# Kernel tuning notes

Hardware: AMD Instinct MI355X
Metric: run time of the kernel (lower is better)

Reference implementation:

```python
import jax, jax.numpy as jnp
import numpy as np

NUM_TAGS = 128
VOCAB = 50257
SEQ_LEN = 8192
START_TAG = 0   # tag2id['<s>'] in the original
END_TAG = 1     # vocab['</s>'] in the original (code quirk; treated as end-tag id)
NEG_INF = -10000.0


def setup_inputs() -> dict:
    key = jax.random.key(0)
    k1, k2, k3 = jax.random.split(key, 3)
    x = jax.random.randint(k1, (SEQ_LEN,), 0, VOCAB)
    emit_score = jax.random.normal(k2, (VOCAB, NUM_TAGS), dtype=jnp.float32)
    transitions = jax.random.normal(k3, (NUM_TAGS, NUM_TAGS), dtype=jnp.float32)
    return {"x": x, "emit_score": emit_score, "transitions": transitions}


def reference(x, emit_score, transitions):
    # CRF forward algorithm (log partition function z).
    # Original: per-timestep, per-tag python loops of log_sum_exp over
    # _score = alphas[:, None] + emit[ch_id][None, :] + transitions.
    # All num_tags updates at step t read the *old* alphas (the in-place
    # writes only touch _score's source after it was built), so this is the
    # standard vectorized recurrence: a logsumexp reduction over the prev-tag axis.
    emits = emit_score[x[1:]]  # [S-1, T] gathered emission scores
    init_alphas = jnp.full((NUM_TAGS,), NEG_INF, dtype=emit_score.dtype).at[START_TAG].set(0.0)

    def step(alphas, emit_t):
        # score[prev, cur] = alphas[prev] + emit_t[cur] + transitions[prev, cur]
        score = alphas[:, None] + emit_t[None, :] + transitions  # [T, T]
        return jax.nn.logsumexp(score, axis=0), None

    alphas, _ = jax.lax.scan(step, init_alphas, emits)
    z = jax.nn.logsumexp(alphas + transitions[:, END_TAG])  # scalar
    return z
```

## Files before the change

kernel.cpp:

```cpp
#include <hip/hip_runtime.h>

#define NTG 128
#define NSTEPS 8191
#define GCH 512
#define LCH 16
#define MATF16 (NTG*NTG)

typedef _Float16 half8v  __attribute__((ext_vector_type(8)));
typedef _Float16 half4v  __attribute__((ext_vector_type(4)));
typedef float    float4v __attribute__((ext_vector_type(4)));

__device__ __forceinline__ int su(int row, int col){
  return (row*NTG + col) ^ ((row & 15) << 3);
}

__device__ __forceinline__ float wave_max(float v){
#pragma unroll
  for (int m = 32; m >= 1; m >>= 1) v = fmaxf(v, __shfl_xor(v, m));
  return v;
}
__device__ __forceinline__ float wave_sum(float v){
#pragma unroll
  for (int m = 32; m >= 1; m >>= 1) v += __shfl_xor(v, m);
  return v;
}

__global__ __launch_bounds__(256, 2)
void k_chunks(const int* __restrict__ x, const float* __restrict__ emit,
              const float* __restrict__ T, _Float16* __restrict__ Pn,
              _Float16* __restrict__ Pt, double* __restrict__ scale)
{
  __shared__ _Float16 X[MATF16];
  __shared__ float red_g[2][4];

  const int t = threadIdx.x;
  const int lane = t & 63, wv = t >> 6;
  const int l15 = lane & 15, g4 = lane >> 4;
  const int g = blockIdx.x;
  const int s0 = g*LCH;
  const int nst = min(LCH, NSTEPS - s0);

  half8v aE[2][4];
#pragma unroll
  for (int jt=0; jt<2; ++jt){
    const int j = (wv*2+jt)*16 + l15;
#pragma unroll
    for (int ks=0; ks<4; ++ks){
      half8v a;
#pragma unroll
      for (int jj=0; jj<8; ++jj)
        a[jj] = (_Float16)__expf(T[(ks*32 + g4*8 + jj)*NTG + j]);
      aE[jt][ks] = a;
    }
  }

  double cacc;
  {
    const int tok = x[1+s0];
    const float* er = emit + (size_t)tok*NTG;
    const float2 me2 = *(const float2*)(er + lane*2);
    const float m0 = wave_max(fmaxf(me2.x, me2.y));
    const float sa = __expf(me2.x - m0) * 0.0078125f;
    const float sb = __expf(me2.y - m0) * 0.0078125f;
    const int j0 = lane*2;
    for (int it2=0; it2<32; ++it2){
      const int idx = it2*256 + t;
      const int i = idx >> 6;
      const float2 tv = *(const float2*)(T + (size_t)i*NTG + j0);
      union { unsigned int u; _Float16 h[2]; } pk;
      pk.h[0] = (_Float16)(__expf(tv.x)*sa);
      pk.h[1] = (_Float16)(__expf(tv.y)*sb);
      *(unsigned int*)&X[su(i, j0)] = pk.u;
    }
    cacc = (double)m0 + 4.852030263919617;
  }
  __syncthreads();

  float pscale = 1.0f;
  float4v accv[2][8];
  for (int s=1; s<nst; ++s){
    const int tok = x[1+s0+s];
    const float* er = emit + (size_t)tok*NTG;
    const float2 me2 = *(const float2*)(er + lane*2);
    const float m = wave_max(fmaxf(me2.x, me2.y));
    float ehp[2][4];
#pragma unroll
    for (int jt=0; jt<2; ++jt)
#pragma unroll
      for (int r=0; r<4; ++r)
        ehp[jt][r] = __expf(er[(wv*2+jt)*16 + g4*4 + r] - m) * pscale;

#pragma unroll
    for (int jt=0; jt<2; ++jt)
#pragma unroll
      for (int it=0; it<8; ++it) accv[jt][it] = (float4v){0.f,0.f,0.f,0.f};

#pragma unroll
    for (int it=0; it<8; ++it){
      const int c = it*16 + l15;
      half8v bf[4];
#pragma unroll
      for (int ks=0; ks<4; ++ks)
        bf[ks] = *(const half8v*)&X[su(c, ks*32 + g4*8)];
#pragma unroll
      for (int jt=0; jt<2; ++jt)
#pragma unroll
        for (int ks=0; ks<4; ++ks)
          accv[jt][it] = __builtin_amdgcn_mfma_f32_16x16x32_f16(aE[jt][ks], bf[ks], accv[jt][it], 0,0,0);
    }

    float gm = 0.f;
#pragma unroll
    for (int jt=0; jt<2; ++jt)
#pragma unroll
      for (int it=0; it<8; ++it)
#pragma unroll
        for (int r=0;r<4;r++){
          const float v = accv[jt][it][r]*ehp[jt][r];
          accv[jt][it][r] = v;
          gm = fmaxf(gm, v);
        }
    __syncthreads();
#pragma unroll
    for (int jt=0; jt<2; ++jt)
#pragma unroll
      for (int it=0; it<8; ++it){
        half4v h;
#pragma unroll
        for (int r=0;r<4;r++) h[r] = (_Float16)accv[jt][it][r];
        *(half4v*)&X[su(it*16 + l15, (wv*2+jt)*16 + g4*4)] = h;
      }
    gm = wave_max(gm);
    if (lane==0) red_g[s&1][wv] = gm;
    __syncthreads();
    const float gmax = fmaxf(fmaxf(red_g[s&1][0],red_g[s&1][1]),
                             fmaxf(red_g[s&1][2],red_g[s&1][3]));
    pscale = 1.0f/gmax;
    cacc += (double)m + (double)__logf(gmax);
  }

  const float inv = pscale;
  unsigned int* pn = (unsigned int*)(Pn + (size_t)g*MATF16);
  unsigned int* pt = (unsigned int*)(Pt + (size_t)g*MATF16);
  for (int it2=0; it2<32; ++it2){
    const int idx = it2*256 + t;
    const int i = idx >> 6, j0 = (t&63)*2;
    union { unsigned int u; _Float16 h[2]; } pk;
    pk.u = *(const unsigned int*)&X[su(i, j0)];
    pk.h[0] = (_Float16)((float)pk.h[0]*inv);
    pk.h[1] = (_Float16)((float)pk.h[1]*inv);
    pn[idx] = pk.u;
  }
  for (int it2=0; it2<32; ++it2){
    const int uidx = it2*256 + t;
    const int jj = uidx >> 6, ii = (t&63)*2;
    union { unsigned int u; _Float16 h[2]; } pk;
    pk.h[0] = (_Float16)((float)X[su(ii,   jj)]*inv);
    pk.h[1] = (_Float16)((float)X[su(ii+1, jj)]*inv);
    pt[uidx] = pk.u;
  }
  if (t==0) scale[g] = cacc;
}

__global__ __launch_bounds__(256, 2)
void k_comb8(const _Float16* __restrict__ Pn_in, const _Float16* __restrict__ Pt_in,
             const double* __restrict__ Sin,
             _Float16* __restrict__ Pn_out, _Float16* __restrict__ Pt_out,
             double* __restrict__ Sout)
{
  __shared__ _Float16 X[MATF16];
  __shared__ float red_g[2][4];
  const int t = threadIdx.x;
  const int lane = t & 63, wv = t >> 6;
  const int l15 = lane & 15, g4 = lane >> 4;
  const int p = blockIdx.x;

  const unsigned int* src = (const unsigned int*)(Pn_in + (size_t)p*8*MATF16);
  for (int it2=0; it2<32; ++it2){
    const int idx = it2*256 + t;
    const int i = idx >> 6, j0 = (t&63)*2;
    *(unsigned int*)&X[su(i, j0)] = src[idx];
  }
  __syncthreads();

  float pscale = 1.0f;
  double slog = 0.0;
  float4v accv[2][8];
  for (int mi=1; mi<8; ++mi){
    const _Float16* Yt = Pt_in + (size_t)(p*8+mi)*MATF16;
    half8v aB[2][4];
#pragma unroll
    for (int jt=0; jt<2; ++jt){
      const int j = (wv*2+jt)*16 + l15;
#pragma unroll
      for (int ks=0; ks<4; ++ks)
        aB[jt][ks] = *(const half8v*)(Yt + (size_t)j*NTG + ks*32 + g4*8);
    }

#pragma unroll
    for (int jt=0; jt<2; ++jt)
#pragma unroll
      for (int it=0; it<8; ++it) accv[jt][it] = (float4v){0.f,0.f,0.f,0.f};

#pragma unroll
    for (int it=0; it<8; ++it){
      const int c = it*16 + l15;
      half8v bf[4];
#pragma unroll
      for (int ks=0; ks<4; ++ks)
        bf[ks] = *(const half8v*)&X[su(c, ks*32 + g4*8)];
#pragma unroll
      for (int jt=0; jt<2; ++jt)
#pragma unroll
        for (int ks=0; ks<4; ++ks)
          accv[jt][it] = __builtin_amdgcn_mfma_f32_16x16x32_f16(aB[jt][ks], bf[ks], accv[jt][it], 0,0,0);
    }

    float gm = 0.f;
#pragma unroll
    for (int jt=0; jt<2; ++jt)
#pragma unroll
      for (int it=0; it<8; ++it)
#pragma unroll
        for (int r=0;r<4;r++){
          const float v = accv[jt][it][r]*pscale;
          accv[jt][it][r] = v;
          gm = fmaxf(gm, v);
        }
    __syncthreads();
#pragma unroll
    for (int jt=0; jt<2; ++jt)
#pragma unroll
      for (int it=0; it<8; ++it){
        half4v h;
#pragma unroll
        for (int r=0;r<4;r++) h[r] = (_Float16)accv[jt][it][r];
        *(half4v*)&X[su(it*16 + l15, (wv*2+jt)*16 + g4*4)] = h;
      }
    gm = wave_max(gm);
    if (lane==0) red_g[mi&1][wv] = gm;
    __syncthreads();
    const float gmax = fmaxf(fmaxf(red_g[mi&1][0],red_g[mi&1][1]),
                             fmaxf(red_g[mi&1][2],red_g[mi&1][3]));
    pscale = 1.0f/gmax;
    slog += (double)__logf(gmax);
  }

  const float inv = pscale;
  unsigned int* pn = (unsigned int*)(Pn_out + (size_t)p*MATF16);
  unsigned int* pt = (unsigned int*)(Pt_out + (size_t)p*MATF16);
  for (int it2=0; it2<32; ++it2){
    const int idx = it2*256 + t;
    const int i = idx >> 6, j0 = (t&63)*2;
    union { unsigned int u; _Float16 h[2]; } pk;
    pk.u = *(const unsigned int*)&X[su(i, j0)];
    pk.h[0] = (_Float16)((float)pk.h[0]*inv);
    pk.h[1] = (_Float16)((float)pk.h[1]*inv);
    pn[idx] = pk.u;
  }
  for (int it2=0; it2<32; ++it2){
    const int uidx = it2*256 + t;
    const int jj = uidx >> 6, ii = (t&63)*2;
    union { unsigned int u; _Float16 h[2]; } pk;
    pk.h[0] = (_Float16)((float)X[su(ii,   jj)]*inv);
    pk.h[1] = (_Float16)((float)X[su(ii+1, jj)]*inv);
    pt[uidx] = pk.u;
  }
  if (t==0){
    double ssum = slog;
#pragma unroll
    for (int q=0;q<8;q++) ssum += Sin[p*8+q];
    Sout[p] = ssum;
  }
}

__global__ void k_final(const _Float16* __restrict__ PtC, const double* __restrict__ scC,
                        const float* __restrict__ T, float* __restrict__ out)
{
  __shared__ float u[2][NTG];
  __shared__ float red[4], red2[4];
  const int t = threadIdx.x;
  const int lane = t & 63, wv = t >> 6;

  double acc = 0.0;
#pragma unroll
  for (int q=0;q<8;q++) acc += scC[q];

  if (t < NTG) u[0][t] = (t==0) ? 1.f : 0.f;
  __syncthreads();

  int cur = 0;
  const int r = t >> 1, off = (t&1)*64;
  for (int k=0;k<8;k++){
    const _Float16* Y = PtC + (size_t)k*MATF16 + (size_t)r*NTG + off;
    float dot = 0.f;
#pragma unroll
    for (int q=0;q<8;q++){
      const half8v h = *(const half8v*)(Y + q*8);
#pragma unroll
      for (int e=0;e<8;e++) dot += (float)h[e]*u[cur][off + q*8 + e];
    }
    dot += __shfl_xor(dot, 1);
    if ((t&1)==0) u[cur^1][r] = dot;
    __syncthreads();
    cur ^= 1;
  }

  const float val = (t < NTG) ? (__logf(u[cur][t]) + T[t*NTG + 1]) : -3.0e38f;
  float mx = wave_max(val);
  if (lane==0) red[wv] = mx;
  __syncthreads();
  mx = fmaxf(fmaxf(red[0],red[1]), fmaxf(red[2],red[3]));
  const float e = (t < NTG) ? __expf(val - mx) : 0.f;
  const float s = wave_sum(e);
  if (lane==0) red2[wv] = s;
  __syncthreads();
  if (t==0){
    const double z = (double)mx + log((double)(red2[0]+red2[1]+red2[2]+red2[3])) + acc;
    out[0] = (float)z;
  }
}

extern "C" void kernel_launch(void* const* d_in, const int* in_sizes, int n_in,
                              void* d_out, int out_size, void* d_ws, size_t ws_size,
                              hipStream_t stream)
{
  const int*   x    = (const int*)d_in[0];
  const float* emit = (const float*)d_in[1];
  const float* T    = (const float*)d_in[2];
  float* out = (float*)d_out;

  _Float16* PnA = (_Float16*)d_ws;
  _Float16* PtA = PnA + (size_t)512*MATF16;
  _Float16* PnB = PtA + (size_t)512*MATF16;
  _Float16* PtB = PnB + (size_t)64*MATF16;
  _Float16* PnC = PtB + (size_t)64*MATF16;
  _Float16* PtC = PnC + (size_t)8*MATF16;
  double* scA = (double*)(PtC + (size_t)8*MATF16);
  double* scB = scA + 512;
  double* scC = scB + 64;

  k_chunks<<<GCH, 256, 0, stream>>>(x, emit, T, PnA, PtA, scA);
  k_comb8<<<64, 256, 0, stream>>>(PnA, PtA, scA, PnB, PtB, scB);
  k_comb8<<< 8, 256, 0, stream>>>(PnB, PtB, scB, PnC, PtC, scC);
  k_final<<<1, 256, 0, stream>>>(PtC, scC, T, out);
}
```

Measured before the change: 181.3 us.

## Precompute exp(T) once, widen blocks to 512 threads, drop redundant Pn stores

Adds a prep kernel that computes exp(transitions) once in fp16, in both normal and transposed layouts, so chunk blocks load these instead of recomputing exps. Chunk and combine kernels move to 512 threads (8 waves, one 16-column tile each), which halves per-wave MFMA work and accumulator registers. The emission scale is folded into the A operand (fp16 multiply) rather than applied to accumulators. The Pn output is removed; combine kernels rebuild their initial state from the transposed Pt via a transposed LDS write. Risks include extra fp16 rounding from pre-scaling A, an added kernel launch, and bank conflicts on the transposed LDS stores.

```diff
diff --git a/kernel.cpp b/kernel.cpp
--- a/kernel.cpp
+++ b/kernel.cpp
@@ -25,13 +25,22 @@
   return v;
 }
 
-__global__ __launch_bounds__(256, 2)
+__global__ void k_prep(const float* __restrict__ T, _Float16* __restrict__ En,
+                       _Float16* __restrict__ Et){
+  const int idx = blockIdx.x*256 + threadIdx.x;
+  const int i = idx >> 7, j = idx & 127;
+  const float v = __expf(T[idx]);
+  En[idx] = (_Float16)v;
+  Et[j*NTG + i] = (_Float16)v;
+}
+
+__global__ __launch_bounds__(512, 4)
 void k_chunks(const int* __restrict__ x, const float* __restrict__ emit,
-              const float* __restrict__ T, _Float16* __restrict__ Pn,
+              const _Float16* __restrict__ Et, const _Float16* __restrict__ En,
               _Float16* __restrict__ Pt, double* __restrict__ scale)
 {
   __shared__ _Float16 X[MATF16];
-  __shared__ float red_g[2][4];
+  __shared__ float red_g[2][8];
 
   const int t = threadIdx.x;
   const int lane = t & 63, wv = t >> 6;
@@ -39,61 +48,50 @@
   const int g = blockIdx.x;
   const int s0 = g*LCH;
   const int nst = min(LCH, NSTEPS - s0);
-
-  half8v aE[2][4];
-#pragma unroll
-  for (int jt=0; jt<2; ++jt){
-    const int j = (wv*2+jt)*16 + l15;
-#pragma unroll
-    for (int ks=0; ks<4; ++ks){
-      half8v a;
-#pragma unroll
-      for (int jj=0; jj<8; ++jj)
-        a[jj] = (_Float16)__expf(T[(ks*32 + g4*8 + jj)*NTG + j]);
-      aE[jt][ks] = a;
-    }
-  }
+  const int jA = wv*16 + l15;
+
+  half8v aE[4];
+#pragma unroll
+  for (int ks=0; ks<4; ++ks)
+    aE[ks] = *(const half8v*)(Et + jA*NTG + ks*32 + g4*8);
 
   double cacc;
   {
     const int tok = x[1+s0];
     const float* er = emit + (size_t)tok*NTG;
-    const float2 me2 = *(const float2*)(er + lane*2);
+    const float2 me2 = *(const float2*)(er + (t&63)*2);
     const float m0 = wave_max(fmaxf(me2.x, me2.y));
     const float sa = __expf(me2.x - m0) * 0.0078125f;
     const float sb = __expf(me2.y - m0) * 0.0078125f;
-    const int j0 = lane*2;
-    for (int it2=0; it2<32; ++it2){
-      const int idx = it2*256 + t;
-      const int i = idx >> 6;
-      const float2 tv = *(const float2*)(T + (size_t)i*NTG + j0);
+    const int j0 = (t&63)*2;
+    const unsigned int* ens = (const unsigned int*)En;
+#pragma unroll
+    for (int it=0; it<16; ++it){
+      const int idx = it*512 + t;
       union { unsigned int u; _Float16 h[2]; } pk;
-      pk.h[0] = (_Float16)(__expf(tv.x)*sa);
-      pk.h[1] = (_Float16)(__expf(tv.y)*sb);
-      *(unsigned int*)&X[su(i, j0)] = pk.u;
+      pk.u = ens[idx];
+      pk.h[0] = (_Float16)((float)pk.h[0]*sa);
+      pk.h[1] = (_Float16)((float)pk.h[1]*sb);
+      *(unsigned int*)&X[su(idx>>6, j0)] = pk.u;
     }
     cacc = (double)m0 + 4.852030263919617;
   }
   __syncthreads();
 
   float pscale = 1.0f;
-  float4v accv[2][8];
+  float4v accv[8];
   for (int s=1; s<nst; ++s){
     const int tok = x[1+s0+s];
     const float* er = emit + (size_t)tok*NTG;
-    const float2 me2 = *(const float2*)(er + lane*2);
+    const float2 me2 = *(const float2*)(er + (t&63)*2);
     const float m = wave_max(fmaxf(me2.x, me2.y));
-    float ehp[2][4];
-#pragma unroll
-    for (int jt=0; jt<2; ++jt)
-#pragma unroll
-      for (int r=0; r<4; ++r)
-        ehp[jt][r] = __expf(er[(wv*2+jt)*16 + g4*4 + r] - m) * pscale;
-
-#pragma unroll
-    for (int jt=0; jt<2; ++jt)
-#pragma unroll
-      for (int it=0; it<8; ++it) accv[jt][it] = (float4v){0.f,0.f,0.f,0.f};
+    const _Float16 hA = (_Float16)(__expf(er[jA] - m) * pscale);
+    half8v ap[4];
+#pragma unroll
+    for (int ks=0; ks<4; ++ks) ap[ks] = aE[ks] * hA;
+
+#pragma unroll
+    for (int it=0; it<8; ++it) accv[it] = (float4v){0.f,0.f,0.f,0.f};
 
 #pragma unroll
     for (int it=0; it<8; ++it){
@@ -103,57 +101,40 @@
       for (int ks=0; ks<4; ++ks)
         bf[ks] = *(const half8v*)&X[su(c, ks*32 + g4*8)];
 #pragma unroll
-      for (int jt=0; jt<2; ++jt)
-#pragma unroll
-        for (int ks=0; ks<4; ++ks)
-          accv[jt][it] = __builtin_amdgcn_mfma_f32_16x16x32_f16(aE[jt][ks], bf[ks], accv[jt][it], 0,0,0);
+      for (int ks=0; ks<4; ++ks)
+        accv[it] = __builtin_amdgcn_mfma_f32_16x16x32_f16(ap[ks], bf[ks], accv[it], 0,0,0);
     }
 
     float gm = 0.f;
 #pragma unroll
-    for (int jt=0; jt<2; ++jt)
-#pragma unroll
-      for (int it=0; it<8; ++it)
-#pragma unroll
-        for (int r=0;r<4;r++){
-          const float v = accv[jt][it][r]*ehp[jt][r];
-          accv[jt][it][r] = v;
-          gm = fmaxf(gm, v);
-        }
-    __syncthreads();
-#pragma unroll
-    for (int jt=0; jt<2; ++jt)
-#pragma unroll
-      for (int it=0; it<8; ++it){
-        half4v h;
-#pragma unroll
-        for (int r=0;r<4;r++) h[r] = (_Float16)accv[jt][it][r];
-        *(half4v*)&X[su(it*16 + l15, (wv*2+jt)*16 + g4*4)] = h;
-      }
+    for (int it=0; it<8; ++it)
+#pragma unroll
+      for (int r=0;r<4;r++) gm = fmaxf(gm, accv[it][r]);
+    __syncthreads();
+#pragma unroll
+    for (int it=0; it<8; ++it){
+      half4v h;
+#pragma unroll
+      for (int r=0;r<4;r++) h[r] = (_Float16)accv[it][r];
+      *(half4v*)&X[su(it*16 + l15, wv*16 + g4*4)] = h;
+    }
     gm = wave_max(gm);
     if (lane==0) red_g[s&1][wv] = gm;
     __syncthreads();
-    const float gmax = fmaxf(fmaxf(red_g[s&1][0],red_g[s&1][1]),
-                             fmaxf(red_g[s&1][2],red_g[s&1][3]));
+    float gmax = red_g[s&1][0];
+#pragma unroll
+    for (int q=1;q<8;q++) gmax = fmaxf(gmax, red_g[s&1][q]);
     pscale = 1.0f/gmax;
     cacc += (double)m + (double)__logf(gmax);
   }
 
   const float inv = pscale;
-  unsigned int* pn = (unsigned int*)(Pn + (size_t)g*MATF16);
   unsigned int* pt = (unsigned int*)(Pt + (size_t)g*MATF16);
-  for (int it2=0; it2<32; ++it2){
-    const int idx = it2*256 + t;
-    const int i = idx >> 6, j0 = (t&63)*2;
-    union { unsigned int u; _Float16 h[2]; } pk;
-    pk.u = *(const unsigned int*)&X[su(i, j0)];
-    pk.h[0] = (_Float16)((float)pk.h[0]*inv);
-    pk.h[1] = (_Float16)((float)pk.h[1]*inv);
-    pn[idx] = pk.u;
-  }
-  for (int it2=0; it2<32; ++it2){
-    const int uidx = it2*256 + t;
-    const int jj = uidx >> 6, ii = (t&63)*2;
+  const int ii = (t&63)*2;
+#pragma unroll
+  for (int it=0; it<16; ++it){
+    const int uidx = it*512 + t;
+    const int jj = uidx >> 6;
     union { unsigned int u; _Float16 h[2]; } pk;
     pk.h[0] = (_Float16)((float)X[su(ii,   jj)]*inv);
     pk.h[1] = (_Float16)((float)X[su(ii+1, jj)]*inv);
@@ -162,45 +143,45 @@
   if (t==0) scale[g] = cacc;
 }
 
-__global__ __launch_bounds__(256, 2)
-void k_comb8(const _Float16* __restrict__ Pn_in, const _Float16* __restrict__ Pt_in,
-             const double* __restrict__ Sin,
-             _Float16* __restrict__ Pn_out, _Float16* __restrict__ Pt_out,
-             double* __restrict__ Sout)
+__global__ __launch_bounds__(512, 2)
+void k_comb8(const _Float16* __restrict__ Pt_in, const double* __restrict__ Sin,
+             _Float16* __restrict__ Pt_out, double* __restrict__ Sout)
 {
   __shared__ _Float16 X[MATF16];
-  __shared__ float red_g[2][4];
+  __shared__ float red_g[2][8];
   const int t = threadIdx.x;
   const int lane = t & 63, wv = t >> 6;
   const int l15 = lane & 15, g4 = lane >> 4;
   const int p = blockIdx.x;
-
-  const unsigned int* src = (const unsigned int*)(Pn_in + (size_t)p*8*MATF16);
-  for (int it2=0; it2<32; ++it2){
-    const int idx = it2*256 + t;
-    const int i = idx >> 6, j0 = (t&63)*2;
-    *(unsigned int*)&X[su(i, j0)] = src[idx];
+  const int jA = wv*16 + l15;
+
+  {
+    const unsigned int* src = (const unsigned int*)(Pt_in + (size_t)p*8*MATF16);
+    const int i0 = (t&63)*2;
+#pragma unroll
+    for (int it=0; it<16; ++it){
+      const int pos = it*512 + t;
+      union { unsigned int u; _Float16 h[2]; } pk;
+      pk.u = src[pos];
+      const int j = pos >> 6;
+      X[su(i0,   j)] = pk.h[0];
+      X[su(i0+1, j)] = pk.h[1];
+    }
   }
   __syncthreads();
 
   float pscale = 1.0f;
   double slog = 0.0;
-  float4v accv[2][8];
+  float4v accv[8];
   for (int mi=1; mi<8; ++mi){
     const _Float16* Yt = Pt_in + (size_t)(p*8+mi)*MATF16;
-    half8v aB[2][4];
-#pragma unroll
-    for (int jt=0; jt<2; ++jt){
-      const int j = (wv*2+jt)*16 + l15;
-#pragma unroll
-      for (int ks=0; ks<4; ++ks)
-        aB[jt][ks] = *(const half8v*)(Yt + (size_t)j*NTG + ks*32 + g4*8);
-    }
-
-#pragma unroll
-    for (int jt=0; jt<2; ++jt)
-#pragma unroll
-      for (int it=0; it<8; ++it) accv[jt][it] = (float4v){0.f,0.f,0.f,0.f};
+    half8v aB[4];
+#pragma unroll
+    for (int ks=0; ks<4; ++ks)
+      aB[ks] = *(const half8v*)(Yt + jA*NTG + ks*32 + g4*8);
+
+#pragma unroll
+    for (int it=0; it<8; ++it) accv[it] = (float4v){0.f,0.f,0.f,0.f};
 
 #pragma unroll
     for (int it=0; it<8; ++it){
@@ -210,57 +191,44 @@
       for (int ks=0; ks<4; ++ks)
         bf[ks] = *(const half8v*)&X[su(c, ks*32 + g4*8)];
 #pragma unroll
-      for (int jt=0; jt<2; ++jt)
-#pragma unroll
-        for (int ks=0; ks<4; ++ks)
-          accv[jt][it] = __builtin_amdgcn_mfma_f32_16x16x32_f16(aB[jt][ks], bf[ks], accv[jt][it], 0,0,0);
+      for (int ks=0; ks<4; ++ks)
+        accv[it] = __builtin_amdgcn_mfma_f32_16x16x32_f16(aB[ks], bf[ks], accv[it], 0,0,0);
     }
 
     float gm = 0.f;
 #pragma unroll
-    for (int jt=0; jt<2; ++jt)
-#pragma unroll
-      for (int it=0; it<8; ++it)
-#pragma unroll
-        for (int r=0;r<4;r++){
-          const float v = accv[jt][it][r]*pscale;
-          accv[jt][it][r] = v;
-          gm = fmaxf(gm, v);
-        }
-    __syncthreads();
-#pragma unroll
-    for (int jt=0; jt<2; ++jt)
-#pragma unroll
-      for (int it=0; it<8; ++it){
-        half4v h;
-#pragma unroll
-        for (int r=0;r<4;r++) h[r] = (_Float16)accv[jt][it][r];
-        *(half4v*)&X[su(it*16 + l15, (wv*2+jt)*16 + g4*4)] = h;
+    for (int it=0; it<8; ++it)
+#pragma unroll
+      for (int r=0;r<4;r++){
+        const float v = accv[it][r]*pscale;
+        accv[it][r] = v;
+        gm = fmaxf(gm, v);
       }
+    __syncthreads();
+#pragma unroll
+    for (int it=0; it<8; ++it){
+      half4v h;
+#pragma unroll
+      for (int r=0;r<4;r++) h[r] = (_Float16)accv[it][r];
+      *(half4v*)&X[su(it*16 + l15, wv*16 + g4*4)] = h;
+    }
     gm = wave_max(gm);
     if (lane==0) red_g[mi&1][wv] = gm;
     __syncthreads();
-    const float gmax = fmaxf(fmaxf(red_g[mi&1][0],red_g[mi&1][1]),
-                             fmaxf(red_g[mi&1][2],red_g[mi&1][3]));
+    float gmax = red_g[mi&1][0];
+#pragma unroll
+    for (int q=1;q<8;q++) gmax = fmaxf(gmax, red_g[mi&1][q]);
     pscale = 1.0f/gmax;
     slog += (double)__logf(gmax);
   }
 
   const float inv = pscale;
-  unsigned int* pn = (unsigned int*)(Pn_out + (size_t)p*MATF16);
   unsigned int* pt = (unsigned int*)(Pt_out + (size_t)p*MATF16);
-  for (int it2=0; it2<32; ++it2){
-    const int idx = it2*256 + t;
-    const int i = idx >> 6, j0 = (t&63)*2;
-    union { unsigned int u; _Float16 h[2]; } pk;
-    pk.u = *(const unsigned int*)&X[su(i, j0)];
-    pk.h[0] = (_Float16)((float)pk.h[0]*inv);
-    pk.h[1] = (_Float16)((float)pk.h[1]*inv);
-    pn[idx] = pk.u;
-  }
-  for (int it2=0; it2<32; ++it2){
-    const int uidx = it2*256 + t;
-    const int jj = uidx >> 6, ii = (t&63)*2;
+  const int ii = (t&63)*2;
+#pragma unroll
+  for (int it=0; it<16; ++it){
+    const int uidx = it*512 + t;
+    const int jj = uidx >> 6;
     union { unsigned int u; _Float16 h[2]; } pk;
     pk.h[0] = (_Float16)((float)X[su(ii,   jj)]*inv);
     pk.h[1] = (_Float16)((float)X[su(ii+1, jj)]*inv);
@@ -330,18 +298,18 @@
   const float* T    = (const float*)d_in[2];
   float* out = (float*)d_out;
 
-  _Float16* PnA = (_Float16*)d_ws;
-  _Float16* PtA = PnA + (size_t)512*MATF16;
-  _Float16* PnB = PtA + (size_t)512*MATF16;
-  _Float16* PtB = PnB + (size_t)64*MATF16;
-  _Float16* PnC = PtB + (size_t)64*MATF16;
-  _Float16* PtC = PnC + (size_t)8*MATF16;
+  _Float16* En  = (_Float16*)d_ws;
+  _Float16* Et  = En  + MATF16;
+  _Float16* PtA = Et  + MATF16;
+  _Float16* PtB = PtA + (size_t)512*MATF16;
+  _Float16* PtC = PtB + (size_t)64*MATF16;
   double* scA = (double*)(PtC + (size_t)8*MATF16);
   double* scB = scA + 512;
   double* scC = scB + 64;
 
-  k_chunks<<<GCH, 256, 0, stream>>>(x, emit, T, PnA, PtA, scA);
-  k_comb8<<<64, 256, 0, stream>>>(PnA, PtA, scA, PnB, PtB, scB);
-  k_comb8<<< 8, 256, 0, stream>>>(PnB, PtB, scB, PnC, PtC, scC);
+  k_prep<<<64, 256, 0, stream>>>(T, En, Et);
+  k_chunks<<<GCH, 512, 0, stream>>>(x, emit, Et, En, PtA, scA);
+  k_comb8<<<64, 512, 0, stream>>>(PtA, scA, PtB, scB);
+  k_comb8<<< 8, 512, 0, stream>>>(PtB, scB, PtC, scC);
   k_final<<<1, 256, 0, stream>>>(PtC, scC, T, out);
 }
```

After: 182.5 us. About the same (+0.6%).
